# Kernel optimization log

Hardware: AMD Instinct MI355X
Metric: run time of the kernel (lower is better)

## Reference

```python
import jax, jax.numpy as jnp
import numpy as np

B, NPG = 64, 512          # graphs, nodes per graph
N_TOTAL = B * NPG
LIG = 128                 # ligand nodes per graph (segment 0); rest are protein (segment 1)
BOX = 40.0                # Angstrom box for random coords -> realistic radius-graph density
INTER_CUTOFF = 10.0       # normalize_coord is identity (scale=1)
INTRA_CUTOFF = 8.0


def setup_inputs() -> dict:
    key = jax.random.key(0)
    X = jax.random.uniform(key, (N_TOTAL, 1, 3), dtype=jnp.float32) * BOX
    batch_id = jnp.repeat(jnp.arange(B, dtype=jnp.int32), NPG)
    local = jnp.tile(jnp.arange(NPG, dtype=jnp.int32), B)
    segment_id = (local >= LIG).astype(jnp.int32)
    is_global = jnp.logical_or(local == 0, local == LIG)  # one global node per segment
    return {"X": X, "batch_id": batch_id, "segment_id": segment_id, "is_global": is_global}


def _radial_edges(X, src_dst, cutoff):
    # src_dst: [E, 2] node indices; X: [N, C, 3], channel 0 holds coords
    p = X[:, 0][src_dst]                              # [E, 2, 3]
    dist = jnp.linalg.norm(p[:, 0] - p[:, 1], axis=-1)
    return src_dst[dist <= cutoff].T                  # [2, E']


def reference(X, batch_id, segment_id, is_global):
    N = batch_id.shape[0]
    nB = int(batch_id[-1]) + 1
    lengths = jax.ops.segment_sum(jnp.ones_like(batch_id), batch_id, num_segments=nB)
    max_n = int(jnp.max(lengths))
    offsets = jnp.concatenate([jnp.zeros((1,), lengths.dtype), jnp.cumsum(lengths)[:-1]])
    gni = jnp.arange(N)
    gni2lni = gni - offsets[batch_id]                 # local node index within its graph

    # Dense [N, max_n] same-batch mask via cumsum trick (O(N*max_n))
    same_bid = jnp.zeros((N, max_n), jnp.float32)
    same_bid = same_bid.at[gni, lengths[batch_id] - 1].set(1.0)
    same_bid = 1.0 - jnp.cumsum(same_bid, axis=-1)
    same_bid = jnp.concatenate([jnp.ones((N, 1), jnp.float32), same_bid[:, :-1]], axis=-1)
    same_bid = same_bid.at[gni, gni2lni].set(0.0)     # remove self edges

    row, col = jnp.nonzero(same_bid)                  # all same-graph candidate pairs
    col = col + offsets[batch_id[row]]                # local col -> global node index

    row_global = is_global[row]
    col_global = is_global[col]
    not_global = jnp.logical_not(jnp.logical_or(row_global, col_global))
    row_seg = segment_id[row]
    col_seg = segment_id[col]

    # intra-protein context edges (segment 1, within 8A)
    sel = (row_seg == col_seg) & (row_seg == 1) & not_global
    ctx_edges = _radial_edges(X, jnp.stack([row[sel], col[sel]], axis=1), INTRA_CUTOFF)

    # inter ligand-protein edges (within 10A)
    sel = (row_seg != col_seg) & not_global
    ir, ic = row[sel], col[sel]
    inter_edges = _radial_edges(X, jnp.stack([ir, ic], axis=1), INTER_CUTOFF)
    if inter_edges.shape[1] == 0:
        inter_edges = jnp.array([[ir[0], ic[0]], [ic[0], ir[0]]], dtype=inter_edges.dtype)

    reduced_inter_edge_batchid = batch_id[inter_edges[0][inter_edges[0] < inter_edges[1]]]
    reduced_inter_edge_offsets = offsets[reduced_inter_edge_batchid]

    # global<->same-segment edges and global<->global edges appended to context
    sel = (row_seg == col_seg) & jnp.logical_not(not_global)
    global_normal = jnp.stack([row[sel], col[sel]])
    sel = row_global & col_global
    global_global = jnp.stack([row[sel], col[sel]])
    ctx_edges = jnp.concatenate([ctx_edges, global_normal, global_global], axis=1)

    return ctx_edges, inter_edges, reduced_inter_edge_batchid, reduced_inter_edge_offsets
```

## Files before the change

### kernel.cpp

```cpp
#include <hip/hip_runtime.h>

#define NB 64
#define NPG 512
#define LIG 128
#define NBLK 512
#define RPB 64

__device__ __forceinline__ float dist2(float dx, float dy, float dz) {
    return __fadd_rn(__fadd_rn(__fmul_rn(dx, dx), __fmul_rn(dy, dy)), __fmul_rn(dz, dz));
}
#define T10 __uint_as_float(0x42C80001u)
#define T8  __uint_as_float(0x42800001u)

__global__ __launch_bounds__(1024) void count_kernel(const float* __restrict__ X,
                                                     unsigned long long* __restrict__ gmask,
                                                     int* __restrict__ bp) {
    __shared__ float s[NPG * 3];
    __shared__ unsigned long long smask[RPB * 8];
    __shared__ int rc[RPB], ri[RPB];
    const int b = blockIdx.x;
    const int g = b >> 3;
    const int o = b & 7;
    const int t = threadIdx.x;
    const int lane = t & 63;
    const int w = t >> 6;
    if (t < 384) ((float4*)s)[t] = ((const float4*)X)[g * 384 + t];
    if (t < 512) smask[t] = 0ull;
    __syncthreads();

    float cx[8], cy[8], cz[8];
#pragma unroll
    for (int k = 0; k < 8; ++k) {
        const int c = k * 64 + lane;
        cx[k] = s[3 * c]; cy[k] = s[3 * c + 1]; cz[k] = s[3 * c + 2];
    }

#pragma unroll
    for (int j = 0; j < 4; ++j) {
        const int lr = w * 4 + j;
        const int r = o * 64 + lr;
        const float px = s[3 * r], py = s[3 * r + 1], pz = s[3 * r + 2];
        int cc = 0, ci = 0;
        if (o < 2) {
            if (r != 0) {
#pragma unroll
                for (int k = 2; k < 8; ++k) {
                    unsigned long long m =
                        __ballot(dist2(px - cx[k], py - cy[k], pz - cz[k]) <= T10);
                    if (k == 2) m &= ~1ull;
                    if (lane == 0) smask[lr * 8 + k] = m;
                    ci += __popcll(m);
                }
            }
        } else if (r != LIG) {
#pragma unroll
            for (int k = 0; k < 2; ++k) {
                unsigned long long m =
                    __ballot(dist2(px - cx[k], py - cy[k], pz - cz[k]) <= T10);
                if (k == 0) m &= ~1ull;
                if (lane == 0) smask[lr * 8 + k] = m;
                ci += __popcll(m);
            }
            const int kr = r >> 6;
            const unsigned long long selfbit = 1ull << (r & 63);
#pragma unroll
            for (int k = 2; k < 8; ++k) {
                unsigned long long m =
                    __ballot(dist2(px - cx[k], py - cy[k], pz - cz[k]) <= T8);
                if (k == 2) m &= ~1ull;
                if (k == kr) m &= ~selfbit;
                if (lane == 0) smask[lr * 8 + k] = m;
                cc += __popcll(m);
            }
        }
        if (lane == 0) { rc[lr] = cc; ri[lr] = ci; }
    }
    __syncthreads();
    if (t < 512) gmask[(size_t)b * 512 + t] = smask[t];
    if (t < 64) {
        int c = rc[t], i = ri[t];
#pragma unroll
        for (int off = 32; off >= 1; off >>= 1) {
            c += __shfl_down(c, off, 64);
            i += __shfl_down(i, off, 64);
        }
        if (t == 0) {
            bp[b] = c;
            bp[NBLK + b] = i;
            bp[2 * NBLK + b] = (o < 2) ? i : 0;
        }
    }
}

__global__ __launch_bounds__(512) void emit_kernel(const unsigned long long* __restrict__ gmask,
                                                   const int* __restrict__ bp,
                                                   int* __restrict__ out) {
    __shared__ unsigned long long smask[RPB * 8];
    __shared__ int sc[RPB], si[RPB], sr[RPB];
    __shared__ int blkb[3], tot[3];
    const int b = blockIdx.x;
    const int g = b >> 3;
    const int o = b & 7;
    const int t = threadIdx.x;
    const int lane = t & 63;
    const int w = t >> 6;
    const unsigned long long lmask = (1ull << lane) - 1ull;
    const int gn = g * NPG;

    smask[t] = gmask[(size_t)b * 512 + t];

    if (w < 3) {
        const int base = w * NBLK + lane * 8;
        int v[8]; int sum = 0;
#pragma unroll
        for (int i = 0; i < 8; ++i) { v[i] = bp[base + i]; sum += v[i]; }
        int incl = sum;
#pragma unroll
        for (int off = 1; off < 64; off <<= 1) {
            int n = __shfl_up(incl, off, 64);
            if (lane >= off) incl += n;
        }
        if (lane == (b >> 3)) {
            int e = incl - sum;
            const int idx = b & 7;
            for (int i = 0; i < idx; ++i) e += v[i];
            blkb[w] = e;
        }
        if (lane == 63) tot[w] = incl;
    }
    __syncthreads();

    if (t < RPB) {
        int mc = 0, mi = 0;
        if (o < 2) {
#pragma unroll
            for (int k = 2; k < 8; ++k) mi += __popcll(smask[t * 8 + k]);
        } else {
            mi = __popcll(smask[t * 8 + 0]) + __popcll(smask[t * 8 + 1]);
#pragma unroll
            for (int k = 2; k < 8; ++k) mc += __popcll(smask[t * 8 + k]);
        }
        const int mr = (o < 2) ? mi : 0;
        int ic = mc, ii = mi, ir = mr;
#pragma unroll
        for (int off = 1; off < 64; off <<= 1) {
            int a0 = __shfl_up(ic, off, 64);
            int a1 = __shfl_up(ii, off, 64);
            int a2 = __shfl_up(ir, off, 64);
            if (lane >= off) { ic += a0; ii += a1; ir += a2; }
        }
        sc[t] = blkb[0] + ic - mc;
        si[t] = blkb[1] + ii - mi;
        sr[t] = blkb[2] + ir - mr;
    }
    __syncthreads();

    const int Eci = tot[0];
    const int Ei  = tot[1];
    const int Er  = tot[2];
    const int Ectx = Eci + NB * 1020 + NB * 2;

    int* ctx_src   = out;
    int* ctx_dst   = out + Ectx;
    int* inter_src = out + 2 * Ectx;
    int* inter_dst = inter_src + Ei;
    int* red_bid   = out + 2 * Ectx + 2 * Ei;
    int* red_off   = red_bid + Er;

    for (int j = 0; j < 8; ++j) {
        const int lr = w * 8 + j;
        const int r = o * 64 + lr;
        const int row = gn + r;

        unsigned long long m[8];
#pragma unroll
        for (int k = 0; k < 8; ++k) m[k] = smask[lr * 8 + k];

        if (o < 2) {
            if (r == 0) {
                for (int k = 0; k < 2; ++k) {
                    const int c = k * 64 + lane;
                    if (c >= 1 && c < LIG) {
                        const int pos = Eci + g * 1020 + (c - 1);
                        ctx_src[pos] = row; ctx_dst[pos] = gn + c;
                    }
                }
                if (lane == 0) {
                    const int pos = Eci + NB * 1020 + g * 2;
                    ctx_src[pos] = row; ctx_dst[pos] = gn + LIG;
                }
            } else {
                int ib = si[lr];
                int rb = sr[lr];
#pragma unroll
                for (int k = 2; k < 8; ++k) {
                    if (m[k]) {
                        if ((m[k] >> lane) & 1ull) {
                            const int c = k * 64 + lane;
                            const int p = __popcll(m[k] & lmask);
                            inter_src[ib + p] = row; inter_dst[ib + p] = gn + c;
                            red_bid[rb + p] = g;     red_off[rb + p] = gn;
                        }
                        const int cnt = __popcll(m[k]);
                        ib += cnt; rb += cnt;
                    }
                }
                if (lane == 0) {
                    const int pos = Eci + g * 1020 + (LIG - 1) + (r - 1);
                    ctx_src[pos] = row; ctx_dst[pos] = gn;
                }
            }
        } else {
            if (r == LIG) {
                for (int k = 2; k < 8; ++k) {
                    const int c = k * 64 + lane;
                    if (c > LIG) {
                        const int pos = Eci + g * 1020 + 2 * (LIG - 1) + (c - LIG - 1);
                        ctx_src[pos] = row; ctx_dst[pos] = gn + c;
                    }
                }
                if (lane == 0) {
                    const int pos = Eci + NB * 1020 + g * 2 + 1;
                    ctx_src[pos] = row; ctx_dst[pos] = gn;
                }
            } else {
                int ib = si[lr];
#pragma unroll
                for (int k = 0; k < 2; ++k) {
                    if (m[k]) {
                        if ((m[k] >> lane) & 1ull) {
                            const int c = k * 64 + lane;
                            const int pos = ib + __popcll(m[k] & lmask);
                            inter_src[pos] = row; inter_dst[pos] = gn + c;
                        }
                        ib += __popcll(m[k]);
                    }
                }
                int cb = sc[lr];
#pragma unroll
                for (int k = 2; k < 8; ++k) {
                    if (m[k]) {
                        if ((m[k] >> lane) & 1ull) {
                            const int c = k * 64 + lane;
                            const int pos = cb + __popcll(m[k] & lmask);
                            ctx_src[pos] = row; ctx_dst[pos] = gn + c;
                        }
                        cb += __popcll(m[k]);
                    }
                }
                if (lane == 0) {
                    const int pos = Eci + g * 1020 + 2 * (LIG - 1) + (NPG - LIG - 1) + (r - LIG - 1);
                    ctx_src[pos] = row; ctx_dst[pos] = gn + LIG;
                }
            }
        }
    }
}

extern "C" void kernel_launch(void* const* d_in, const int* in_sizes, int n_in,
                              void* d_out, int out_size, void* d_ws, size_t ws_size,
                              hipStream_t stream) {
    (void)in_sizes; (void)n_in; (void)out_size; (void)ws_size;
    const float* X = (const float*)d_in[0];
    int* ws = (int*)d_ws;
    int* bp = ws;
    unsigned long long* gmask =
        (unsigned long long*)(ws + 4096);
    int* out = (int*)d_out;

    count_kernel<<<NBLK, 1024, 0, stream>>>(X, gmask, bp);
    emit_kernel<<<NBLK, 512, 0, stream>>>(gmask, bp, out);
}
```

Before: 81.83 us.

## Split work into 1024 blocks of 32 rows and batch reduced-edge writes

Halves the rows per block and the block size, giving 1024 blocks of 512 threads for both kernels, so the GPU has more blocks to spread across compute units. Mask stores in count_kernel are batched into one lane-0 write loop per row. The reduced-inter batch-id and offset outputs become a contiguous fill per block instead of scattered per-edge writes. The cost is a larger prefix scan over per-block counts (16 values per lane), more redundant coordinate loads into shared memory, and the scan now depends on exact block indexing.

```diff
diff --git a/kernel.cpp b/kernel.cpp
--- a/kernel.cpp
+++ b/kernel.cpp
@@ -3,8 +3,9 @@
 #define NB 64
 #define NPG 512
 #define LIG 128
-#define NBLK 512
-#define RPB 64
+#define NBLK 1024
+#define RPB 32
+#define THREADS 512
 
 __device__ __forceinline__ float dist2(float dx, float dy, float dz) {
     return __fadd_rn(__fadd_rn(__fmul_rn(dx, dx), __fmul_rn(dy, dy)), __fmul_rn(dz, dz));
@@ -12,20 +13,20 @@
 #define T10 __uint_as_float(0x42C80001u)
 #define T8  __uint_as_float(0x42800001u)
 
-__global__ __launch_bounds__(1024) void count_kernel(const float* __restrict__ X,
-                                                     unsigned long long* __restrict__ gmask,
-                                                     int* __restrict__ bp) {
+__global__ __launch_bounds__(THREADS) void count_kernel(const float* __restrict__ X,
+                                                        unsigned long long* __restrict__ gmask,
+                                                        int* __restrict__ bp) {
     __shared__ float s[NPG * 3];
     __shared__ unsigned long long smask[RPB * 8];
     __shared__ int rc[RPB], ri[RPB];
     const int b = blockIdx.x;
-    const int g = b >> 3;
-    const int o = b & 7;
+    const int g = b >> 4;
+    const int h = b & 15;
     const int t = threadIdx.x;
     const int lane = t & 63;
     const int w = t >> 6;
     if (t < 384) ((float4*)s)[t] = ((const float4*)X)[g * 384 + t];
-    if (t < 512) smask[t] = 0ull;
+    if (t < RPB * 8) smask[t] = 0ull;
     __syncthreads();
 
     float cx[8], cy[8], cz[8];
@@ -38,27 +39,33 @@
 #pragma unroll
     for (int j = 0; j < 4; ++j) {
         const int lr = w * 4 + j;
-        const int r = o * 64 + lr;
+        const int r = h * 32 + lr;
         const float px = s[3 * r], py = s[3 * r + 1], pz = s[3 * r + 2];
         int cc = 0, ci = 0;
-        if (o < 2) {
+        if (h < 4) {
             if (r != 0) {
+                unsigned long long mm[6];
 #pragma unroll
                 for (int k = 2; k < 8; ++k) {
                     unsigned long long m =
                         __ballot(dist2(px - cx[k], py - cy[k], pz - cz[k]) <= T10);
                     if (k == 2) m &= ~1ull;
-                    if (lane == 0) smask[lr * 8 + k] = m;
+                    mm[k - 2] = m;
                     ci += __popcll(m);
                 }
+                if (lane == 0) {
+#pragma unroll
+                    for (int k = 0; k < 6; ++k) smask[lr * 8 + 2 + k] = mm[k];
+                }
             }
         } else if (r != LIG) {
+            unsigned long long mm[8];
 #pragma unroll
             for (int k = 0; k < 2; ++k) {
                 unsigned long long m =
                     __ballot(dist2(px - cx[k], py - cy[k], pz - cz[k]) <= T10);
                 if (k == 0) m &= ~1ull;
-                if (lane == 0) smask[lr * 8 + k] = m;
+                mm[k] = m;
                 ci += __popcll(m);
             }
             const int kr = r >> 6;
@@ -69,16 +76,21 @@
                     __ballot(dist2(px - cx[k], py - cy[k], pz - cz[k]) <= T8);
                 if (k == 2) m &= ~1ull;
                 if (k == kr) m &= ~selfbit;
-                if (lane == 0) smask[lr * 8 + k] = m;
+                mm[k] = m;
                 cc += __popcll(m);
             }
+            if (lane == 0) {
+#pragma unroll
+                for (int k = 0; k < 8; ++k) smask[lr * 8 + k] = mm[k];
+            }
         }
         if (lane == 0) { rc[lr] = cc; ri[lr] = ci; }
     }
     __syncthreads();
-    if (t < 512) gmask[(size_t)b * 512 + t] = smask[t];
+    if (t < RPB * 8) gmask[(size_t)b * (RPB * 8) + t] = smask[t];
     if (t < 64) {
-        int c = rc[t], i = ri[t];
+        int c = (t < RPB) ? rc[t] : 0;
+        int i = (t < RPB) ? ri[t] : 0;
 #pragma unroll
         for (int off = 32; off >= 1; off >>= 1) {
             c += __shfl_down(c, off, 64);
@@ -87,42 +99,42 @@
         if (t == 0) {
             bp[b] = c;
             bp[NBLK + b] = i;
-            bp[2 * NBLK + b] = (o < 2) ? i : 0;
-        }
-    }
-}
-
-__global__ __launch_bounds__(512) void emit_kernel(const unsigned long long* __restrict__ gmask,
-                                                   const int* __restrict__ bp,
-                                                   int* __restrict__ out) {
+            bp[2 * NBLK + b] = (h < 4) ? i : 0;
+        }
+    }
+}
+
+__global__ __launch_bounds__(THREADS) void emit_kernel(const unsigned long long* __restrict__ gmask,
+                                                       const int* __restrict__ bp,
+                                                       int* __restrict__ out) {
     __shared__ unsigned long long smask[RPB * 8];
-    __shared__ int sc[RPB], si[RPB], sr[RPB];
-    __shared__ int blkb[3], tot[3];
+    __shared__ int sc[RPB], si[RPB];
+    __shared__ int blkb[3], tot[3], sint;
     const int b = blockIdx.x;
-    const int g = b >> 3;
-    const int o = b & 7;
+    const int g = b >> 4;
+    const int h = b & 15;
     const int t = threadIdx.x;
     const int lane = t & 63;
     const int w = t >> 6;
     const unsigned long long lmask = (1ull << lane) - 1ull;
     const int gn = g * NPG;
 
-    smask[t] = gmask[(size_t)b * 512 + t];
+    if (t < RPB * 8) smask[t] = gmask[(size_t)b * (RPB * 8) + t];
 
     if (w < 3) {
-        const int base = w * NBLK + lane * 8;
-        int v[8]; int sum = 0;
-#pragma unroll
-        for (int i = 0; i < 8; ++i) { v[i] = bp[base + i]; sum += v[i]; }
+        const int base = w * NBLK + lane * 16;
+        int v[16]; int sum = 0;
+#pragma unroll
+        for (int i = 0; i < 16; ++i) { v[i] = bp[base + i]; sum += v[i]; }
         int incl = sum;
 #pragma unroll
         for (int off = 1; off < 64; off <<= 1) {
             int n = __shfl_up(incl, off, 64);
             if (lane >= off) incl += n;
         }
-        if (lane == (b >> 3)) {
+        if (lane == (b >> 4)) {
             int e = incl - sum;
-            const int idx = b & 7;
+            const int idx = b & 15;
             for (int i = 0; i < idx; ++i) e += v[i];
             blkb[w] = e;
         }
@@ -132,7 +144,7 @@
 
     if (t < RPB) {
         int mc = 0, mi = 0;
-        if (o < 2) {
+        if (h < 4) {
 #pragma unroll
             for (int k = 2; k < 8; ++k) mi += __popcll(smask[t * 8 + k]);
         } else {
@@ -140,18 +152,16 @@
 #pragma unroll
             for (int k = 2; k < 8; ++k) mc += __popcll(smask[t * 8 + k]);
         }
-        const int mr = (o < 2) ? mi : 0;
-        int ic = mc, ii = mi, ir = mr;
-#pragma unroll
-        for (int off = 1; off < 64; off <<= 1) {
+        int ic = mc, ii = mi;
+#pragma unroll
+        for (int off = 1; off < 32; off <<= 1) {
             int a0 = __shfl_up(ic, off, 64);
             int a1 = __shfl_up(ii, off, 64);
-            int a2 = __shfl_up(ir, off, 64);
-            if (lane >= off) { ic += a0; ii += a1; ir += a2; }
+            if (lane >= off) { ic += a0; ii += a1; }
         }
         sc[t] = blkb[0] + ic - mc;
         si[t] = blkb[1] + ii - mi;
-        sr[t] = blkb[2] + ir - mr;
+        if (t == RPB - 1) sint = ii;
     }
     __syncthreads();
 
@@ -167,16 +177,16 @@
     int* red_bid   = out + 2 * Ectx + 2 * Ei;
     int* red_off   = red_bid + Er;
 
-    for (int j = 0; j < 8; ++j) {
-        const int lr = w * 8 + j;
-        const int r = o * 64 + lr;
+    for (int j = 0; j < 4; ++j) {
+        const int lr = w * 4 + j;
+        const int r = h * 32 + lr;
         const int row = gn + r;
 
         unsigned long long m[8];
 #pragma unroll
         for (int k = 0; k < 8; ++k) m[k] = smask[lr * 8 + k];
 
-        if (o < 2) {
+        if (h < 4) {
             if (r == 0) {
                 for (int k = 0; k < 2; ++k) {
                     const int c = k * 64 + lane;
@@ -191,7 +201,6 @@
                 }
             } else {
                 int ib = si[lr];
-                int rb = sr[lr];
 #pragma unroll
                 for (int k = 2; k < 8; ++k) {
                     if (m[k]) {
@@ -199,10 +208,8 @@
                             const int c = k * 64 + lane;
                             const int p = __popcll(m[k] & lmask);
                             inter_src[ib + p] = row; inter_dst[ib + p] = gn + c;
-                            red_bid[rb + p] = g;     red_off[rb + p] = gn;
                         }
-                        const int cnt = __popcll(m[k]);
-                        ib += cnt; rb += cnt;
+                        ib += __popcll(m[k]);
                     }
                 }
                 if (lane == 0) {
@@ -253,6 +260,15 @@
                     ctx_src[pos] = row; ctx_dst[pos] = gn + LIG;
                 }
             }
+        }
+    }
+
+    if (h < 4) {
+        const int rb0 = blkb[2];
+        const int n = sint;
+        for (int i = t; i < n; i += THREADS) {
+            red_bid[rb0 + i] = g;
+            red_off[rb0 + i] = gn;
         }
     }
 }
@@ -268,6 +284,6 @@
         (unsigned long long*)(ws + 4096);
     int* out = (int*)d_out;
 
-    count_kernel<<<NBLK, 1024, 0, stream>>>(X, gmask, bp);
-    emit_kernel<<<NBLK, 512, 0, stream>>>(gmask, bp, out);
-}
+    count_kernel<<<NBLK, THREADS, 0, stream>>>(X, gmask, bp);
+    emit_kernel<<<NBLK, THREADS, 0, stream>>>(gmask, bp, out);
+}
```

Result: no change. 80.45 us (median of 2 runs) (-1.7%).
